# Kernel optimization log

Measured on AMD Instinct MI355X. Metric: run time of the kernel, lower is better.

Reference implementation:

```python
import jax, jax.numpy as jnp
import numpy as np

# bitsandbytes NF4 codebook (16 quantile values in [-1, 1])
NF4 = jnp.array([
    -1.0, -0.6961928009986877, -0.5250730514526367, -0.39491748809814453,
    -0.28444138169288635, -0.18477343022823334, -0.09105003625154495, 0.0,
    0.07958029955625534, 0.16093020141124725, 0.24611230194568634,
    0.33791524171829224, 0.44070982933044434, 0.5626170039176941,
    0.7229568362236328, 1.0], dtype=jnp.float32)
BLOCK = 64  # bnb default quantization blocksize


def dequant_nf4(codes, absmax):
    """codes: int array of 4-bit indices, absmax: per-64-elem-block scale."""
    flat = NF4[codes.reshape(-1)]                      # codebook lookup
    flat = flat.reshape(-1, BLOCK) * absmax[:, None]   # per-block rescale
    return flat.reshape(codes.shape)


def setup_inputs() -> dict:
    key = jax.random.key(0)
    k1, k2, k3, k4, k5 = jax.random.split(key, 5)
    B, S, IN, OUT, R = 4, 2048, 4096, 4096, 8
    x = jax.random.normal(k1, (B, S, IN), dtype=jnp.float32)
    codes_A = jax.random.randint(k2, (R, IN), 0, 16, dtype=jnp.int32)
    absmax_A = jax.random.uniform(k3, (R * IN // BLOCK,), dtype=jnp.float32)
    codes_B = jax.random.randint(k4, (OUT, R), 0, 16, dtype=jnp.int32)
    absmax_B = jax.random.uniform(k5, (OUT * R // BLOCK,), dtype=jnp.float32)
    return {"x": x, "codes_A": codes_A, "absmax_A": absmax_A,
            "codes_B": codes_B, "absmax_B": absmax_B}


def reference(x, codes_A, absmax_A, codes_B, absmax_B):
    SCALING = 32.0 / 8.0  # alpha / rank
    W_A = dequant_nf4(codes_A, absmax_A)   # [rank, in]
    W_B = dequant_nf4(codes_B, absmax_B)   # [out, rank]
    interm = jnp.einsum('bsi,ri->bsr', x, W_A)          # lora_A: x @ W_A^T
    out = jnp.einsum('bsr,or->bso', interm, W_B)        # lora_B
    return out * SCALING
```

## Files before the change

kernel.cpp:

```cpp
#include <hip/hip_runtime.h>


static __device__ __constant__ float NF4_TBL[16] = {
    -1.0f, -0.6961928009986877f, -0.5250730514526367f, -0.39491748809814453f,
    -0.28444138169288635f, -0.18477343022823334f, -0.09105003625154495f, 0.0f,
    0.07958029955625534f, 0.16093020141124725f, 0.24611230194568634f,
    0.33791524171829224f, 0.44070982933044434f, 0.5626170039176941f,
    0.7229568362236328f, 1.0f};

__global__ void nf4_dequant_kernel(const int* __restrict__ codesA,
                                   const float* __restrict__ absA,
                                   const int* __restrict__ codesB,
                                   const float* __restrict__ absB,
                                   float* __restrict__ wA,
                                   float* __restrict__ wBt,
                                   int n) {
    int id = blockIdx.x * blockDim.x + threadIdx.x;
    if (id < n) {
        wA[id] = NF4_TBL[codesA[id] & 15] * absA[id >> 6];
        const int o = id >> 3;
        const int r = id & 7;
        wBt[r * 4096 + o] = NF4_TBL[codesB[id] & 15] * absB[id >> 6];
    }
}

__global__ __launch_bounds__(256, 4) void lora_a_kernel(
    const float* __restrict__ x,
    const float* __restrict__ wA,
    float* __restrict__ interm) {
    constexpr int IN4 = 4096 / 4;

    const int t    = threadIdx.x;
    const int wave = t >> 6;
    const int lane = t & 63;
    const int r0   = blockIdx.x * 8 + 2 * wave;

    const float4* __restrict__ x0  = (const float4*)(x + (size_t)r0 * 4096);
    const float4* __restrict__ x1  = (const float4*)(x + (size_t)(r0 + 1) * 4096);
    const float4* __restrict__ wA4 = (const float4*)wA;

    float acc0[8], acc1[8];
    #pragma unroll
    for (int r = 0; r < 8; ++r) { acc0[r] = 0.f; acc1[r] = 0.f; }

    #pragma unroll 4
    for (int c = 0; c < 16; ++c) {
        const int idx = lane + 64 * c;
        const float4 xa = x0[idx];
        const float4 xb = x1[idx];
        #pragma unroll
        for (int r = 0; r < 8; ++r) {
            const float4 w = wA4[r * IN4 + idx];
            acc0[r] += xa.x * w.x + xa.y * w.y + xa.z * w.z + xa.w * w.w;
            acc1[r] += xb.x * w.x + xb.y * w.y + xb.z * w.z + xb.w * w.w;
        }
    }

    #pragma unroll
    for (int r = 0; r < 8; ++r) {
        float v0 = acc0[r], v1 = acc1[r];
        #pragma unroll
        for (int off = 32; off > 0; off >>= 1) {
            v0 += __shfl_down(v0, off, 64);
            v1 += __shfl_down(v1, off, 64);
        }
        if (lane == 0) {
            interm[(size_t)r0 * 8 + r]       = v0 * 4.0f;
            interm[(size_t)(r0 + 1) * 8 + r] = v1 * 4.0f;
        }
    }
}

__global__ __launch_bounds__(256, 8) void lora_b_kernel(
    const float* __restrict__ interm,
    const float* __restrict__ wBt,
    float* __restrict__ out) {
    const int t    = threadIdx.x;
    const int row0 = blockIdx.x * 4;

    float im[4][8];
    const float* __restrict__ ip = interm + (size_t)row0 * 8;
    #pragma unroll
    for (int m = 0; m < 4; ++m)
        #pragma unroll
        for (int r = 0; r < 8; ++r)
            im[m][r] = ip[m * 8 + r];

    const float4* __restrict__ wt = (const float4*)wBt;

    #pragma unroll
    for (int k = 0; k < 4; ++k) {
        const int og = t + 256 * k;
        float4 w[8];
        #pragma unroll
        for (int r = 0; r < 8; ++r) w[r] = wt[r * 1024 + og];

        #pragma unroll
        for (int m = 0; m < 4; ++m) {
            float4 s;
            s.x = im[m][0] * w[0].x + im[m][1] * w[1].x + im[m][2] * w[2].x
                + im[m][3] * w[3].x + im[m][4] * w[4].x + im[m][5] * w[5].x
                + im[m][6] * w[6].x + im[m][7] * w[7].x;
            s.y = im[m][0] * w[0].y + im[m][1] * w[1].y + im[m][2] * w[2].y
                + im[m][3] * w[3].y + im[m][4] * w[4].y + im[m][5] * w[5].y
                + im[m][6] * w[6].y + im[m][7] * w[7].y;
            s.z = im[m][0] * w[0].z + im[m][1] * w[1].z + im[m][2] * w[2].z
                + im[m][3] * w[3].z + im[m][4] * w[4].z + im[m][5] * w[5].z
                + im[m][6] * w[6].z + im[m][7] * w[7].z;
            s.w = im[m][0] * w[0].w + im[m][1] * w[1].w + im[m][2] * w[2].w
                + im[m][3] * w[3].w + im[m][4] * w[4].w + im[m][5] * w[5].w
                + im[m][6] * w[6].w + im[m][7] * w[7].w;
            ((float4*)(out + (size_t)(row0 + m) * 4096))[og] = s;
        }
    }
}

extern "C" void kernel_launch(void* const* d_in, const int* in_sizes, int n_in,
                              void* d_out, int out_size, void* d_ws, size_t ws_size,
                              hipStream_t stream) {
    const float* x        = (const float*)d_in[0];
    const int*   codes_A  = (const int*)d_in[1];
    const float* absmax_A = (const float*)d_in[2];
    const int*   codes_B  = (const int*)d_in[3];
    const float* absmax_B = (const float*)d_in[4];
    float* out = (float*)d_out;

    constexpr int NW = 8 * 4096;
    float* wA     = (float*)d_ws;
    float* wBt    = (float*)d_ws + NW;
    float* interm = (float*)d_ws + 2 * NW;

    nf4_dequant_kernel<<<(NW + 255) / 256, 256, 0, stream>>>(
        codes_A, absmax_A, codes_B, absmax_B, wA, wBt, NW);

    lora_a_kernel<<<8192 / 8, 256, 0, stream>>>(x, wA, interm);
    lora_b_kernel<<<8192 / 4, 256, 0, stream>>>(interm, wBt, out);
}
```

Baseline: 258.2 us.

## Fuse LoRA A and B projections into one kernel via shared-memory intermediate

Merges the lora_A reduction and lora_B expansion into a single kernel where each block computes 8 rows' rank-8 intermediates, reduces across two half-IN waves through shared memory, then writes output rows. Removes the global interm round trip and a kernel launch, and reworks the A phase so each wave handles 4 rows over half the input dimension for more x reuse of wA loads. Also makes the transposed W_B dequant writes coalesced. Risks higher register pressure and serialization of read and write phases within a block.

```diff
diff --git a/kernel.cpp b/kernel.cpp
--- a/kernel.cpp
+++ b/kernel.cpp
@@ -18,99 +18,113 @@
     int id = blockIdx.x * blockDim.x + threadIdx.x;
     if (id < n) {
         wA[id] = NF4_TBL[codesA[id] & 15] * absA[id >> 6];
-        const int o = id >> 3;
-        const int r = id & 7;
-        wBt[r * 4096 + o] = NF4_TBL[codesB[id] & 15] * absB[id >> 6];
+        const int r = id >> 12;
+        const int o = id & 4095;
+        wBt[id] = NF4_TBL[codesB[o * 8 + r] & 15] * absB[o >> 3];
     }
 }
 
-__global__ __launch_bounds__(256, 4) void lora_a_kernel(
+__global__ __launch_bounds__(256, 4) void lora_fused_kernel(
     const float* __restrict__ x,
     const float* __restrict__ wA,
-    float* __restrict__ interm) {
-    constexpr int IN4 = 4096 / 4;
+    const float* __restrict__ wBt,
+    float* __restrict__ out) {
+    __shared__ __align__(16) float interm_s[2][8][8];
 
     const int t    = threadIdx.x;
     const int wave = t >> 6;
     const int lane = t & 63;
-    const int r0   = blockIdx.x * 8 + 2 * wave;
+    const int rh   = wave >> 1;
+    const int ih   = wave & 1;
+    const int row0 = blockIdx.x * 8;
 
-    const float4* __restrict__ x0  = (const float4*)(x + (size_t)r0 * 4096);
-    const float4* __restrict__ x1  = (const float4*)(x + (size_t)(r0 + 1) * 4096);
+    const float4* __restrict__ x4  =
+        (const float4*)(x + (size_t)(row0 + rh * 4) * 4096);
     const float4* __restrict__ wA4 = (const float4*)wA;
 
-    float acc0[8], acc1[8];
+    float acc[4][8];
     #pragma unroll
-    for (int r = 0; r < 8; ++r) { acc0[r] = 0.f; acc1[r] = 0.f; }
+    for (int m = 0; m < 4; ++m)
+        #pragma unroll
+        for (int r = 0; r < 8; ++r) acc[m][r] = 0.f;
 
-    #pragma unroll 4
-    for (int c = 0; c < 16; ++c) {
-        const int idx = lane + 64 * c;
-        const float4 xa = x0[idx];
-        const float4 xb = x1[idx];
+    #pragma unroll 2
+    for (int c = 0; c < 8; ++c) {
+        const int idx = ih * 512 + lane + 64 * c;
+        const float4 xa0 = x4[idx];
+        const float4 xa1 = x4[1024 + idx];
+        const float4 xa2 = x4[2048 + idx];
+        const float4 xa3 = x4[3072 + idx];
         #pragma unroll
         for (int r = 0; r < 8; ++r) {
-            const float4 w = wA4[r * IN4 + idx];
-            acc0[r] += xa.x * w.x + xa.y * w.y + xa.z * w.z + xa.w * w.w;
-            acc1[r] += xb.x * w.x + xb.y * w.y + xb.z * w.z + xb.w * w.w;
+            const float4 w = wA4[r * 1024 + idx];
+            acc[0][r] += xa0.x * w.x + xa0.y * w.y + xa0.z * w.z + xa0.w * w.w;
+            acc[1][r] += xa1.x * w.x + xa1.y * w.y + xa1.z * w.z + xa1.w * w.w;
+            acc[2][r] += xa2.x * w.x + xa2.y * w.y + xa2.z * w.z + xa2.w * w.w;
+            acc[3][r] += xa3.x * w.x + xa3.y * w.y + xa3.z * w.z + xa3.w * w.w;
         }
     }
 
     #pragma unroll
-    for (int r = 0; r < 8; ++r) {
-        float v0 = acc0[r], v1 = acc1[r];
+    for (int m = 0; m < 4; ++m) {
         #pragma unroll
-        for (int off = 32; off > 0; off >>= 1) {
-            v0 += __shfl_down(v0, off, 64);
-            v1 += __shfl_down(v1, off, 64);
-        }
-        if (lane == 0) {
-            interm[(size_t)r0 * 8 + r]       = v0 * 4.0f;
-            interm[(size_t)(r0 + 1) * 8 + r] = v1 * 4.0f;
+        for (int r = 0; r < 8; ++r) {
+            float v = acc[m][r];
+            v += __shfl_down(v, 32, 64);
+            v += __shfl_down(v, 16, 64);
+            v += __shfl_down(v, 8, 64);
+            v += __shfl_down(v, 4, 64);
+            v += __shfl_down(v, 2, 64);
+            v += __shfl_down(v, 1, 64);
+            if (lane == 0) interm_s[ih][rh * 4 + m][r] = v;
         }
     }
-}
-
-__global__ __launch_bounds__(256, 8) void lora_b_kernel(
-    const float* __restrict__ interm,
-    const float* __restrict__ wBt,
-    float* __restrict__ out) {
-    const int t    = threadIdx.x;
-    const int row0 = blockIdx.x * 4;
-
-    float im[4][8];
-    const float* __restrict__ ip = interm + (size_t)row0 * 8;
-    #pragma unroll
-    for (int m = 0; m < 4; ++m)
-        #pragma unroll
-        for (int r = 0; r < 8; ++r)
-            im[m][r] = ip[m * 8 + r];
+    __syncthreads();
 
     const float4* __restrict__ wt = (const float4*)wBt;
+    const float4* s0 = (const float4*)&interm_s[0][0][0];
+    const float4* s1 = (const float4*)&interm_s[1][0][0];
 
-    #pragma unroll
-    for (int k = 0; k < 4; ++k) {
-        const int og = t + 256 * k;
-        float4 w[8];
-        #pragma unroll
-        for (int r = 0; r < 8; ++r) w[r] = wt[r * 1024 + og];
-
+    #pragma unroll 1
+    for (int h = 0; h < 2; ++h) {
+        float im[4][8];
         #pragma unroll
         for (int m = 0; m < 4; ++m) {
-            float4 s;
-            s.x = im[m][0] * w[0].x + im[m][1] * w[1].x + im[m][2] * w[2].x
-                + im[m][3] * w[3].x + im[m][4] * w[4].x + im[m][5] * w[5].x
-                + im[m][6] * w[6].x + im[m][7] * w[7].x;
-            s.y = im[m][0] * w[0].y + im[m][1] * w[1].y + im[m][2] * w[2].y
-                + im[m][3] * w[3].y + im[m][4] * w[4].y + im[m][5] * w[5].y
-                + im[m][6] * w[6].y + im[m][7] * w[7].y;
-            s.z = im[m][0] * w[0].z + im[m][1] * w[1].z + im[m][2] * w[2].z
-                + im[m][3] * w[3].z + im[m][4] * w[4].z + im[m][5] * w[5].z
-                + im[m][6] * w[6].z + im[m][7] * w[7].z;
-            s.w = im[m][0] * w[0].w + im[m][1] * w[1].w + im[m][2] * w[2].w
-                + im[m][3] * w[3].w + im[m][4] * w[4].w + im[m][5] * w[5].w
-                + im[m][6] * w[6].w + im[m][7] * w[7].w;
-            ((float4*)(out + (size_t)(row0 + m) * 4096))[og] = s;
+            #pragma unroll
+            for (int j = 0; j < 2; ++j) {
+                const int q = (h * 4 + m) * 2 + j;
+                const float4 a = s0[q];
+                const float4 b = s1[q];
+                im[m][4 * j + 0] = (a.x + b.x) * 4.0f;
+                im[m][4 * j + 1] = (a.y + b.y) * 4.0f;
+                im[m][4 * j + 2] = (a.z + b.z) * 4.0f;
+                im[m][4 * j + 3] = (a.w + b.w) * 4.0f;
+            }
+        }
+        #pragma unroll
+        for (int k = 0; k < 4; ++k) {
+            const int og = t + 256 * k;
+            float4 w[8];
+            #pragma unroll
+            for (int r = 0; r < 8; ++r) w[r] = wt[r * 1024 + og];
+
+            #pragma unroll
+            for (int m = 0; m < 4; ++m) {
+                float4 s;
+                s.x = im[m][0] * w[0].x + im[m][1] * w[1].x + im[m][2] * w[2].x
+                    + im[m][3] * w[3].x + im[m][4] * w[4].x + im[m][5] * w[5].x
+                    + im[m][6] * w[6].x + im[m][7] * w[7].x;
+                s.y = im[m][0] * w[0].y + im[m][1] * w[1].y + im[m][2] * w[2].y
+                    + im[m][3] * w[3].y + im[m][4] * w[4].y + im[m][5] * w[5].y
+                    + im[m][6] * w[6].y + im[m][7] * w[7].y;
+                s.z = im[m][0] * w[0].z + im[m][1] * w[1].z + im[m][2] * w[2].z
+                    + im[m][3] * w[3].z + im[m][4] * w[4].z + im[m][5] * w[5].z
+                    + im[m][6] * w[6].z + im[m][7] * w[7].z;
+                s.w = im[m][0] * w[0].w + im[m][1] * w[1].w + im[m][2] * w[2].w
+                    + im[m][3] * w[3].w + im[m][4] * w[4].w + im[m][5] * w[5].w
+                    + im[m][6] * w[6].w + im[m][7] * w[7].w;
+                ((float4*)(out + (size_t)(row0 + h * 4 + m) * 4096))[og] = s;
+            }
         }
     }
 }
@@ -126,13 +140,11 @@
     float* out = (float*)d_out;
 
     constexpr int NW = 8 * 4096;
-    float* wA     = (float*)d_ws;
-    float* wBt    = (float*)d_ws + NW;
-    float* interm = (float*)d_ws + 2 * NW;
+    float* wA  = (float*)d_ws;
+    float* wBt = (float*)d_ws + NW;
 
     nf4_dequant_kernel<<<(NW + 255) / 256, 256, 0, stream>>>(
         codes_A, absmax_A, codes_B, absmax_B, wA, wBt, NW);
 
-    lora_a_kernel<<<8192 / 8, 256, 0, stream>>>(x, wA, interm);
-    lora_b_kernel<<<8192 / 4, 256, 0, stream>>>(interm, wBt, out);
+    lora_fused_kernel<<<8192 / 8, 256, 0, stream>>>(x, wA, wBt, out);
 }
```

New measurement: 297.1 us. 1.15x slower.

## Fuse LoRA A and B kernels via shared-memory intermediate

Applied to the files above, without the earlier changes.

Merges the lora_A reduction and lora_B expansion into one kernel: each block reduces 8 rows of x against W_A, stores the 8x8 intermediate in shared memory, then writes the 8 output rows. This removes one kernel launch and the global round-trip of the intermediate, and lets the write phase of one block overlap with the read phase of another. The dequant kernel is also changed so wBt writes are coalesced and the gathers go to codes_B instead. The risk is a longer per-block critical path and a barrier between phases, plus more live registers for the 8x8 intermediate.

```diff
diff --git a/kernel.cpp b/kernel.cpp
--- a/kernel.cpp
+++ b/kernel.cpp
@@ -18,25 +18,27 @@
     int id = blockIdx.x * blockDim.x + threadIdx.x;
     if (id < n) {
         wA[id] = NF4_TBL[codesA[id] & 15] * absA[id >> 6];
-        const int o = id >> 3;
-        const int r = id & 7;
-        wBt[r * 4096 + o] = NF4_TBL[codesB[id] & 15] * absB[id >> 6];
+        const int r = id >> 12;
+        const int o = id & 4095;
+        wBt[id] = NF4_TBL[codesB[o * 8 + r] & 15] * absB[o >> 3];
     }
 }
 
-__global__ __launch_bounds__(256, 4) void lora_a_kernel(
+__global__ __launch_bounds__(256, 4) void lora_fused_kernel(
     const float* __restrict__ x,
     const float* __restrict__ wA,
-    float* __restrict__ interm) {
-    constexpr int IN4 = 4096 / 4;
+    const float* __restrict__ wBt,
+    float* __restrict__ out) {
+    __shared__ float interm_s[8][8];
 
     const int t    = threadIdx.x;
     const int wave = t >> 6;
     const int lane = t & 63;
-    const int r0   = blockIdx.x * 8 + 2 * wave;
+    const int row0 = blockIdx.x * 8;
+    const int r0   = row0 + 2 * wave;
 
     const float4* __restrict__ x0  = (const float4*)(x + (size_t)r0 * 4096);
-    const float4* __restrict__ x1  = (const float4*)(x + (size_t)(r0 + 1) * 4096);
+    const float4* __restrict__ x1  = x0 + 1024;
     const float4* __restrict__ wA4 = (const float4*)wA;
 
     float acc0[8], acc1[8];
@@ -50,7 +52,7 @@
         const float4 xb = x1[idx];
         #pragma unroll
         for (int r = 0; r < 8; ++r) {
-            const float4 w = wA4[r * IN4 + idx];
+            const float4 w = wA4[r * 1024 + idx];
             acc0[r] += xa.x * w.x + xa.y * w.y + xa.z * w.z + xa.w * w.w;
             acc1[r] += xb.x * w.x + xb.y * w.y + xb.z * w.z + xb.w * w.w;
         }
@@ -65,30 +67,25 @@
             v1 += __shfl_down(v1, off, 64);
         }
         if (lane == 0) {
-            interm[(size_t)r0 * 8 + r]       = v0 * 4.0f;
-            interm[(size_t)(r0 + 1) * 8 + r] = v1 * 4.0f;
+            interm_s[2 * wave][r]     = v0;
+            interm_s[2 * wave + 1][r] = v1;
         }
     }
-}
+    __syncthreads();
 
-__global__ __launch_bounds__(256, 8) void lora_b_kernel(
-    const float* __restrict__ interm,
-    const float* __restrict__ wBt,
-    float* __restrict__ out) {
-    const int t    = threadIdx.x;
-    const int row0 = blockIdx.x * 4;
-
-    float im[4][8];
-    const float* __restrict__ ip = interm + (size_t)row0 * 8;
+    float ims[8][8];
     #pragma unroll
-    for (int m = 0; m < 4; ++m)
+    for (int m = 0; m < 8; ++m)
         #pragma unroll
-        for (int r = 0; r < 8; ++r)
-            im[m][r] = ip[m * 8 + r];
+        for (int r = 0; r < 8; ++r) {
+            const float v = interm_s[m][r] * 4.0f;
+            ims[m][r] = __int_as_float(
+                __builtin_amdgcn_readfirstlane(__float_as_int(v)));
+        }
 
     const float4* __restrict__ wt = (const float4*)wBt;
 
-    #pragma unroll
+    #pragma unroll 1
     for (int k = 0; k < 4; ++k) {
         const int og = t + 256 * k;
         float4 w[8];
@@ -96,20 +93,20 @@
         for (int r = 0; r < 8; ++r) w[r] = wt[r * 1024 + og];
 
         #pragma unroll
-        for (int m = 0; m < 4; ++m) {
+        for (int m = 0; m < 8; ++m) {
             float4 s;
-            s.x = im[m][0] * w[0].x + im[m][1] * w[1].x + im[m][2] * w[2].x
-                + im[m][3] * w[3].x + im[m][4] * w[4].x + im[m][5] * w[5].x
-                + im[m][6] * w[6].x + im[m][7] * w[7].x;
-            s.y = im[m][0] * w[0].y + im[m][1] * w[1].y + im[m][2] * w[2].y
-                + im[m][3] * w[3].y + im[m][4] * w[4].y + im[m][5] * w[5].y
-                + im[m][6] * w[6].y + im[m][7] * w[7].y;
-            s.z = im[m][0] * w[0].z + im[m][1] * w[1].z + im[m][2] * w[2].z
-                + im[m][3] * w[3].z + im[m][4] * w[4].z + im[m][5] * w[5].z
-                + im[m][6] * w[6].z + im[m][7] * w[7].z;
-            s.w = im[m][0] * w[0].w + im[m][1] * w[1].w + im[m][2] * w[2].w
-                + im[m][3] * w[3].w + im[m][4] * w[4].w + im[m][5] * w[5].w
-                + im[m][6] * w[6].w + im[m][7] * w[7].w;
+            s.x = ims[m][0] * w[0].x + ims[m][1] * w[1].x + ims[m][2] * w[2].x
+                + ims[m][3] * w[3].x + ims[m][4] * w[4].x + ims[m][5] * w[5].x
+                + ims[m][6] * w[6].x + ims[m][7] * w[7].x;
+            s.y = ims[m][0] * w[0].y + ims[m][1] * w[1].y + ims[m][2] * w[2].y
+                + ims[m][3] * w[3].y + ims[m][4] * w[4].y + ims[m][5] * w[5].y
+                + ims[m][6] * w[6].y + ims[m][7] * w[7].y;
+            s.z = ims[m][0] * w[0].z + ims[m][1] * w[1].z + ims[m][2] * w[2].z
+                + ims[m][3] * w[3].z + ims[m][4] * w[4].z + ims[m][5] * w[5].z
+                + ims[m][6] * w[6].z + ims[m][7] * w[7].z;
+            s.w = ims[m][0] * w[0].w + ims[m][1] * w[1].w + ims[m][2] * w[2].w
+                + ims[m][3] * w[3].w + ims[m][4] * w[4].w + ims[m][5] * w[5].w
+                + ims[m][6] * w[6].w + ims[m][7] * w[7].w;
             ((float4*)(out + (size_t)(row0 + m) * 4096))[og] = s;
         }
     }
@@ -126,13 +123,11 @@
     float* out = (float*)d_out;
 
     constexpr int NW = 8 * 4096;
-    float* wA     = (float*)d_ws;
-    float* wBt    = (float*)d_ws + NW;
-    float* interm = (float*)d_ws + 2 * NW;
+    float* wA  = (float*)d_ws;
+    float* wBt = (float*)d_ws + NW;
 
     nf4_dequant_kernel<<<(NW + 255) / 256, 256, 0, stream>>>(
         codes_A, absmax_A, codes_B, absmax_B, wA, wBt, NW);
 
-    lora_a_kernel<<<8192 / 8, 256, 0, stream>>>(x, wA, interm);
-    lora_b_kernel<<<8192 / 4, 256, 0, stream>>>(interm, wBt, out);
+    lora_fused_kernel<<<8192 / 8, 256, 0, stream>>>(x, wA, wBt, out);
 }
```

Result: slower. 360.1 us (+39.5%).
